# Kernel optimization log

Hardware: AMD Instinct MI355X
Metric: run time of the kernel (lower is better)

The kernel has to match this reference:

```python
import jax, jax.numpy as jnp
import numpy as np

N = 50000       # nodes
E = 1600000     # edges (avg degree 32)
F_IN = 128      # input node features
HID = 64        # hidden_dim
H = 2           # heads in conv1
NEG_SLOPE = 0.2 # PyG GATConv default


def gat_conv(x, W, a_src, a_dst, b, src, dst, heads, out_ch):
    """PyG-style GATConv (concat=True). x:[n,f], W:[f,heads*out_ch],
    a_src/a_dst:[heads,out_ch], b:[heads*out_ch], src/dst:[e]."""
    n = x.shape[0]
    xh = (x @ W).reshape(n, heads, out_ch)              # [n,H,C]
    s_src = jnp.sum(xh * a_src[None], axis=-1)          # [n,H]
    s_dst = jnp.sum(xh * a_dst[None], axis=-1)          # [n,H]
    e = jax.nn.leaky_relu(s_src[src] + s_dst[dst], NEG_SLOPE)  # [e,H]
    # segment softmax over incoming edges of each destination node
    emax = jax.ops.segment_max(e, dst, num_segments=n)  # [n,H]
    emax = jnp.where(jnp.isfinite(emax), emax, 0.0)
    p = jnp.exp(e - emax[dst])
    denom = jax.ops.segment_sum(p, dst, num_segments=n)
    alpha = p / (denom[dst] + 1e-16)                    # [e,H]
    out = jax.ops.segment_sum(xh[src] * alpha[..., None], dst, num_segments=n)
    return out.reshape(n, heads * out_ch) + b


def setup_inputs() -> dict:
    key = jax.random.key(0)
    ks = jax.random.split(key, 14)
    g = lambda k, shape, fan: jax.random.normal(k, shape, jnp.float32) / np.sqrt(fan).astype(np.float32)
    return {
        "x": jax.random.normal(ks[0], (N, F_IN), jnp.float32),
        "edge_index": jax.random.randint(ks[1], (2, E), 0, N, jnp.int32),
        "W1": g(ks[2], (F_IN, H * HID), F_IN),
        "a_src1": g(ks[3], (H, HID), HID),
        "a_dst1": g(ks[4], (H, HID), HID),
        "b1": jnp.zeros((H * HID,), jnp.float32),
        "W2": g(ks[5], (H * HID, HID), H * HID),
        "a_src2": g(ks[6], (1, HID), HID),
        "a_dst2": g(ks[7], (1, HID), HID),
        "b2": jnp.zeros((HID,), jnp.float32),
        "Wm": g(ks[8], (HID, 1), HID),
        "bm": jnp.zeros((1,), jnp.float32),
        "Wl": g(ks[9], (HID, 4), HID),
        "bl": jnp.zeros((4,), jnp.float32),
    }


def reference(x, edge_index, W1, a_src1, a_dst1, b1, W2, a_src2, a_dst2, b2, Wm, bm, Wl, bl):
    n = x.shape[0]
    loop = jnp.arange(n, dtype=edge_index.dtype)        # PyG add_self_loops=True
    src = jnp.concatenate([edge_index[0], loop])
    dst = jnp.concatenate([edge_index[1], loop])
    h = jax.nn.relu(gat_conv(x, W1, a_src1, a_dst1, b1, src, dst, H, HID))
    # dropout layers are identity in eval mode
    h = jax.nn.relu(gat_conv(h, W2, a_src2, a_dst2, b2, src, dst, 1, HID))
    mortality = h @ Wm + bm   # [n,1]
    los = h @ Wl + bl         # [n,4]
    return (mortality, los)
```

## Files before the change

### kernel.cpp

```cpp
#include <hip/hip_runtime.h>
#include <hip/hip_bf16.h>

typedef __hip_bfloat16 bf16;
typedef unsigned short ushort_t;
typedef __attribute__((ext_vector_type(8))) short short8;
typedef __attribute__((ext_vector_type(4))) float f32x4;

static __device__ __forceinline__ float b2f(const bf16 v){ return __bfloat162float(v); }
static __device__ __forceinline__ float lrelu(float x){ return x > 0.f ? x : 0.2f * x; }

static __device__ __forceinline__ float ldf(const void* p, size_t i, int f32){
  return f32 ? ((const float*)p)[i] : __bfloat162float(((const bf16*)p)[i]);
}

static __device__ __forceinline__ float wsum(float v){
#pragma unroll
  for (int o = 32; o; o >>= 1) v += __shfl_xor(v, o, 64);
  return v;
}
static __device__ __forceinline__ float wmax(float v){
#pragma unroll
  for (int o = 32; o; o >>= 1) v = fmaxf(v, __shfl_xor(v, o, 64));
  return v;
}
static __device__ __forceinline__ float qsum(float v){
  v += __shfl_xor(v, 1); v += __shfl_xor(v, 2);
  v += __shfl_xor(v, 4); v += __shfl_xor(v, 8);
  return v;
}

static __device__ __forceinline__ unsigned short f2bf(float x){
  unsigned u = __float_as_uint(x);
  unsigned r = (u + 0x7fffu + ((u >> 16) & 1u)) >> 16;
  return (unsigned short)r;
}
static __device__ __forceinline__ float bfval(unsigned short h){
  return __uint_as_float(((unsigned)h) << 16);
}
static __device__ __forceinline__ unsigned packbf2(float a, float b){
  return ((unsigned)f2bf(b) << 16) | (unsigned)f2bf(a);
}
static __device__ __forceinline__ float unlo(unsigned v){ return __uint_as_float(v << 16); }
static __device__ __forceinline__ float unhi(unsigned v){ return __uint_as_float(v & 0xffff0000u); }

__global__ void k_detect(const unsigned short* __restrict__ x, int* __restrict__ flag){
  __shared__ int cnt;
  if (threadIdx.x == 0) cnt = 0;
  __syncthreads();
  int bad = 0;
  for (int i = threadIdx.x; i < 8192; i += 256){
    int e = (x[i] >> 7) & 0xFF;
    if (e >= 133) bad++;
  }
  atomicAdd(&cnt, bad);
  __syncthreads();
  if (threadIdx.x == 0) *flag = (cnt > 16) ? 1 : 0;
}

__global__ void k_zero(int* __restrict__ p, int n){
  int i = blockIdx.x * blockDim.x + threadIdx.x;
  if (i < n) p[i] = 0;
}

#define CHUNK 8192

__global__ __launch_bounds__(256) void k_bincount(const int* __restrict__ ei,
                                                  int* __restrict__ bucketCnt,
                                                  int E, int Etot, int nbuck){
  __shared__ int lcnt[256];
  int t = threadIdx.x;
  lcnt[t] = 0;
  __syncthreads();
  int base = blockIdx.x * CHUNK;
#pragma unroll
  for (int k = 0; k < CHUNK / 256; k++){
    int i = base + k * 256 + t;
    if (i < Etot){
      int dst = (i < E) ? ei[E + i] : (i - E);
      atomicAdd(&lcnt[dst >> 8], 1);
    }
  }
  __syncthreads();
  if (t < nbuck && lcnt[t]) atomicAdd(&bucketCnt[t], lcnt[t]);
}

__global__ __launch_bounds__(256) void k_bucketscan(const int* __restrict__ bucketCnt,
                                                    int* __restrict__ bucketBase,
                                                    int* __restrict__ bucketCur, int nbuck){
  __shared__ int sm[256];
  int t = threadIdx.x;
  int v = (t < nbuck) ? bucketCnt[t] : 0;
  sm[t] = v;
  __syncthreads();
#pragma unroll
  for (int o = 1; o < 256; o <<= 1){
    int x = (t >= o) ? sm[t - o] : 0;
    __syncthreads();
    sm[t] += x;
    __syncthreads();
  }
  int excl = sm[t] - v;
  if (t < nbuck){ bucketBase[t] = excl; bucketCur[t] = excl; }
  if (t == 255) bucketBase[nbuck] = sm[255];
}

__global__ __launch_bounds__(256) void k_binscatter(const int* __restrict__ ei,
                                                    int* __restrict__ bucketCur,
                                                    unsigned* __restrict__ binned,
                                                    int E, int Etot, int nbuck){
  __shared__ int lcnt[256];
  __shared__ int lcur[256];
  int t = threadIdx.x;
  lcnt[t] = 0;
  __syncthreads();
  int base = blockIdx.x * CHUNK;
#pragma unroll
  for (int k = 0; k < CHUNK / 256; k++){
    int i = base + k * 256 + t;
    if (i < Etot){
      int dst = (i < E) ? ei[E + i] : (i - E);
      atomicAdd(&lcnt[dst >> 8], 1);
    }
  }
  __syncthreads();
  if (t < nbuck) lcur[t] = lcnt[t] ? atomicAdd(&bucketCur[t], lcnt[t]) : 0;
  __syncthreads();
#pragma unroll
  for (int k = 0; k < CHUNK / 256; k++){
    int i = base + k * 256 + t;
    if (i < Etot){
      int src, dst;
      if (i < E){ src = ei[i]; dst = ei[E + i]; } else { src = i - E; dst = i - E; }
      int p = atomicAdd(&lcur[dst >> 8], 1);
      binned[p] = (unsigned)src | ((unsigned)(dst & 255) << 24);
    }
  }
}

#define SORTCAP 12288
__global__ __launch_bounds__(256) void k_bucketsort(const int* __restrict__ bucketBase,
                                                    const unsigned* __restrict__ binned,
                                                    int* __restrict__ deg, int* __restrict__ offs,
                                                    int* __restrict__ csr, int N){
  __shared__ int lcnt[256];
  __shared__ int lsc[256];
  __shared__ int lcur[256];
  __shared__ int lsrc[SORTCAP];
  int t = threadIdx.x;
  int b = blockIdx.x;
  int s0 = bucketBase[b], s1 = bucketBase[b + 1];
  int cnt = s1 - s0;
  int node0 = b << 8;
  lcnt[t] = 0;
  __syncthreads();
  for (int i = t; i < cnt; i += 256){
    unsigned v = binned[s0 + i];
    atomicAdd(&lcnt[v >> 24], 1);
  }
  __syncthreads();
  lsc[t] = lcnt[t];
  __syncthreads();
#pragma unroll
  for (int o = 1; o < 256; o <<= 1){
    int x = (t >= o) ? lsc[t - o] : 0;
    __syncthreads();
    lsc[t] += x;
    __syncthreads();
  }
  int excl = lsc[t] - lcnt[t];
  int node = node0 + t;
  if (node < N){ deg[node] = lcnt[t]; offs[node] = s0 + excl; }
  lcur[t] = excl;
  __syncthreads();
  if (cnt <= SORTCAP){
    for (int i = t; i < cnt; i += 256){
      unsigned v = binned[s0 + i];
      int p = atomicAdd(&lcur[v >> 24], 1);
      lsrc[p] = (int)(v & 0xFFFFFFu);
    }
    __syncthreads();
    for (int i = t; i < cnt; i += 256) csr[s0 + i] = lsrc[i];
  } else {
    for (int i = t; i < cnt; i += 256){
      unsigned v = binned[s0 + i];
      int p = atomicAdd(&lcur[v >> 24], 1);
      csr[s0 + p] = (int)(v & 0xFFFFFFu);
    }
  }
}

__global__ __launch_bounds__(256) void k_prepw(const void* __restrict__ W, int ncol, int nct,
                                               const int* __restrict__ flagp,
                                               unsigned short* __restrict__ hi,
                                               unsigned short* __restrict__ lo){
  const int f = *flagp;
  int t = blockIdx.x * 256 + threadIdx.x;
  int j = t & 7;
  int lane = (t >> 3) & 63;
  int ct = (t >> 9) % nct;
  int kc = t / (512 * nct);
  int k = kc * 32 + ((lane >> 4) << 3) + j;
  int col = ct * 16 + (lane & 15);
  float w = ldf(W, (size_t)k * ncol + col, f);
  unsigned short h = f2bf(w);
  hi[t] = h;
  lo[t] = f2bf(w - bfval(h));
}

__global__ __launch_bounds__(256) void k_gemm1m(
    const void* __restrict__ x,
    const unsigned short* __restrict__ whi, const unsigned short* __restrict__ wlo,
    const void* __restrict__ a_src1, const void* __restrict__ a_dst1,
    const int* __restrict__ flagp,
    unsigned* __restrict__ xh1p, float* __restrict__ ssrc1, float* __restrict__ sdst1, int n){
  const int f = *flagp;
  int t = threadIdx.x;
  int lane = t & 63, w = t >> 6;
  int c16 = lane & 15, quad = lane >> 4;
  int nbw = blockIdx.x * 64 + w * 16;
  int an = min(nbw + c16, n - 1);
  f32x4 acc[8];
#pragma unroll
  for (int ct = 0; ct < 8; ct++)
#pragma unroll
    for (int r = 0; r < 4; r++) acc[ct][r] = 0.f;

#pragma unroll
  for (int kc = 0; kc < 4; kc++){
    float av[8];
    short8 ahi, alo;
    if (f){
      const float* row = (const float*)x + (size_t)an * 128 + kc * 32 + quad * 8;
      float4 v0 = *(const float4*)row;
      float4 v1 = *(const float4*)(row + 4);
      av[0] = v0.x; av[1] = v0.y; av[2] = v0.z; av[3] = v0.w;
      av[4] = v1.x; av[5] = v1.y; av[6] = v1.z; av[7] = v1.w;
#pragma unroll
      for (int j = 0; j < 8; j++){
        unsigned short h = f2bf(av[j]);
        ahi[j] = (short)h;
        alo[j] = (short)f2bf(av[j] - bfval(h));
      }
    } else {
      const unsigned short* row = (const unsigned short*)x + (size_t)an * 128 + kc * 32 + quad * 8;
      uint4 v = *(const uint4*)row;
      ahi[0] = (short)(v.x & 0xffff); ahi[1] = (short)(v.x >> 16);
      ahi[2] = (short)(v.y & 0xffff); ahi[3] = (short)(v.y >> 16);
      ahi[4] = (short)(v.z & 0xffff); ahi[5] = (short)(v.z >> 16);
      ahi[6] = (short)(v.w & 0xffff); ahi[7] = (short)(v.w >> 16);
#pragma unroll
      for (int j = 0; j < 8; j++) alo[j] = 0;
    }
#pragma unroll
    for (int ct = 0; ct < 8; ct++){
      const short8 bhi = *(const short8*)(whi + (((size_t)(kc * 8 + ct) * 64 + lane) << 3));
      const short8 blo = *(const short8*)(wlo + (((size_t)(kc * 8 + ct) * 64 + lane) << 3));
      acc[ct] = __builtin_amdgcn_mfma_f32_16x16x32_bf16(ahi, blo, acc[ct], 0, 0, 0);
      acc[ct] = __builtin_amdgcn_mfma_f32_16x16x32_bf16(alo, bhi, acc[ct], 0, 0, 0);
      acc[ct] = __builtin_amdgcn_mfma_f32_16x16x32_bf16(ahi, bhi, acc[ct], 0, 0, 0);
    }
  }

  float as[8], ad[8];
#pragma unroll
  for (int ct = 0; ct < 8; ct++){
    as[ct] = ldf(a_src1, ct * 16 + c16, f);
    ad[ct] = ldf(a_dst1, ct * 16 + c16, f);
  }
  float vs0[4], vs1[4], vd0[4], vd1[4];
#pragma unroll
  for (int r = 0; r < 4; r++){
    float s0 = 0.f, s1 = 0.f, d0 = 0.f, d1 = 0.f;
#pragma unroll
    for (int ct = 0; ct < 4; ct++){
      s0 += acc[ct][r] * as[ct];      d0 += acc[ct][r] * ad[ct];
      s1 += acc[ct + 4][r] * as[ct + 4]; d1 += acc[ct + 4][r] * ad[ct + 4];
    }
    vs0[r] = qsum(s0); vs1[r] = qsum(s1);
    vd0[r] = qsum(d0); vd1[r] = qsum(d1);
  }
#pragma unroll
  for (int r = 0; r < 4; r++){
    int node = nbw + quad * 4 + r;
    if (node < n){
#pragma unroll
      for (int ct = 0; ct < 4; ct++)
        xh1p[(size_t)node * 64 + ct * 16 + c16] = packbf2(acc[ct][r], acc[ct + 4][r]);
    }
  }
  if (c16 == 0){
#pragma unroll
    for (int r = 0; r < 4; r++){
      int node = nbw + quad * 4 + r;
      if (node < n){
        ssrc1[node * 2]     = vs0[r];
        ssrc1[node * 2 + 1] = vs1[r];
        sdst1[node * 2]     = vd0[r];
        sdst1[node * 2 + 1] = vd1[r];
      }
    }
  }
}

__global__ __launch_bounds__(256) void k_gemm2m(
    const float* __restrict__ h1,
    const unsigned short* __restrict__ whi, const unsigned short* __restrict__ wlo,
    const void* __restrict__ a_src2, const void* __restrict__ a_dst2,
    const int* __restrict__ flagp,
    unsigned short* __restrict__ xh2b, float* __restrict__ ssrc2, float* __restrict__ sdst2, int n){
  const int f = *flagp;
  int t = threadIdx.x;
  int lane = t & 63, w = t >> 6;
  int c16 = lane & 15, quad = lane >> 4;
  int nbw = blockIdx.x * 64 + w * 16;
  int an = min(nbw + c16, n - 1);
  f32x4 acc[4];
#pragma unroll
  for (int ct = 0; ct < 4; ct++)
#pragma unroll
    for (int r = 0; r < 4; r++) acc[ct][r] = 0.f;

#pragma unroll
  for (int kc = 0; kc < 4; kc++){
    const float* row = h1 + (size_t)an * 128 + kc * 32 + quad * 8;
    float4 v0 = *(const float4*)row;
    float4 v1 = *(const float4*)(row + 4);
    float av[8] = {v0.x, v0.y, v0.z, v0.w, v1.x, v1.y, v1.z, v1.w};
    short8 ahi, alo;
#pragma unroll
    for (int j = 0; j < 8; j++){
      unsigned short h = f2bf(av[j]);
      ahi[j] = (short)h;
      alo[j] = (short)f2bf(av[j] - bfval(h));
    }
#pragma unroll
    for (int ct = 0; ct < 4; ct++){
      const short8 bhi = *(const short8*)(whi + (((size_t)(kc * 4 + ct) * 64 + lane) << 3));
      const short8 blo = *(const short8*)(wlo + (((size_t)(kc * 4 + ct) * 64 + lane) << 3));
      acc[ct] = __builtin_amdgcn_mfma_f32_16x16x32_bf16(ahi, blo, acc[ct], 0, 0, 0);
      acc[ct] = __builtin_amdgcn_mfma_f32_16x16x32_bf16(alo, bhi, acc[ct], 0, 0, 0);
      acc[ct] = __builtin_amdgcn_mfma_f32_16x16x32_bf16(ahi, bhi, acc[ct], 0, 0, 0);
    }
  }

  float as[4], ad[4];
#pragma unroll
  for (int ct = 0; ct < 4; ct++){
    as[ct] = ldf(a_src2, ct * 16 + c16, f);
    ad[ct] = ldf(a_dst2, ct * 16 + c16, f);
  }
  float vs[4], vd[4];
#pragma unroll
  for (int r = 0; r < 4; r++){
    float s = 0.f, d = 0.f;
#pragma unroll
    for (int ct = 0; ct < 4; ct++){
      s += acc[ct][r] * as[ct];
      d += acc[ct][r] * ad[ct];
    }
    vs[r] = qsum(s); vd[r] = qsum(d);
  }
#pragma unroll
  for (int r = 0; r < 4; r++){
    int node = nbw + quad * 4 + r;
    if (node < n){
#pragma unroll
      for (int ct = 0; ct < 4; ct++)
        xh2b[(size_t)node * 64 + ct * 16 + c16] = f2bf(acc[ct][r]);
    }
  }
  if (c16 == 0){
#pragma unroll
    for (int r = 0; r < 4; r++){
      int node = nbw + quad * 4 + r;
      if (node < n){ ssrc2[node] = vs[r]; sdst2[node] = vd[r]; }
    }
  }
}

__global__ __launch_bounds__(256) void k_agg1(
    const int* __restrict__ offs, const int* __restrict__ deg, const int* __restrict__ csr,
    const float2* __restrict__ ssrc, const float2* __restrict__ sdst,
    const unsigned* __restrict__ xh1p, const void* __restrict__ b1,
    const int* __restrict__ flagp, float* __restrict__ h1, int n){
  int wid = (int)(((size_t)blockIdx.x * blockDim.x + threadIdx.x) >> 6);
  int lane = threadIdx.x & 63;
  if (wid >= n) return;
  int st = offs[wid], d = deg[wid];
  int half = lane >> 5, u = lane & 31;
  float2 sd = sdst[wid];
  const uint2* xp = (const uint2*)xh1p;
  float m0 = -3e38f, m1 = -3e38f, Z0 = 0.f, Z1 = 0.f;
  float a0x = 0.f, a0y = 0.f, a1x = 0.f, a1y = 0.f;
  for (int base = 0; base < d; base += 64){
    int idx = base + lane;
    bool val = idx < d;
    int s = csr[st + (val ? idx : 0)];
    float2 sv = ssrc[s];
    float e0 = val ? lrelu(sv.x + sd.x) : -3e38f;
    float e1 = val ? lrelu(sv.y + sd.y) : -3e38f;
    float nm0 = fmaxf(m0, wmax(e0));
    float nm1 = fmaxf(m1, wmax(e1));
    float r0 = __expf(m0 - nm0), r1 = __expf(m1 - nm1);
    Z0 *= r0; a0x *= r0; a0y *= r0;
    Z1 *= r1; a1x *= r1; a1y *= r1;
    m0 = nm0; m1 = nm1;
    float p0 = val ? __expf(e0 - m0) : 0.f;
    float p1 = val ? __expf(e1 - m1) : 0.f;
    Z0 += wsum(p0); Z1 += wsum(p1);
    int cnt = min(64, d - base);
    int pairs = (cnt + 1) >> 1;
    for (int pj = 0; pj < pairs; pj += 4){
      int jj0 = ((pj + 0) << 1) + half;
      int jj1 = ((pj + 1) << 1) + half;
      int jj2 = ((pj + 2) << 1) + half;
      int jj3 = ((pj + 3) << 1) + half;
      int s0 = __shfl(s, jj0), s1 = __shfl(s, jj1), s2 = __shfl(s, jj2), s3 = __shfl(s, jj3);
      float q00 = __shfl(p0, jj0), q01 = __shfl(p0, jj1), q02 = __shfl(p0, jj2), q03 = __shfl(p0, jj3);
      float q10 = __shfl(p1, jj0), q11 = __shfl(p1, jj1), q12 = __shfl(p1, jj2), q13 = __shfl(p1, jj3);
      uint2 v0 = xp[(size_t)(unsigned)s0 * 32 + u];
      uint2 v1 = xp[(size_t)(unsigned)s1 * 32 + u];
      uint2 v2 = xp[(size_t)(unsigned)s2 * 32 + u];
      uint2 v3 = xp[(size_t)(unsigned)s3 * 32 + u];
      a0x = fmaf(q00, unlo(v0.x), a0x); a0y = fmaf(q00, unlo(v0.y), a0y);
      a1x = fmaf(q10, unhi(v0.x), a1x); a1y = fmaf(q10, unhi(v0.y), a1y);
      a0x = fmaf(q01, unlo(v1.x), a0x); a0y = fmaf(q01, unlo(v1.y), a0y);
      a1x = fmaf(q11, unhi(v1.x), a1x); a1y = fmaf(q11, unhi(v1.y), a1y);
      a0x = fmaf(q02, unlo(v2.x), a0x); a0y = fmaf(q02, unlo(v2.y), a0y);
      a1x = fmaf(q12, unhi(v2.x), a1x); a1y = fmaf(q12, unhi(v2.y), a1y);
      a0x = fmaf(q03, unlo(v3.x), a0x); a0y = fmaf(q03, unlo(v3.y), a0y);
      a1x = fmaf(q13, unhi(v3.x), a1x); a1y = fmaf(q13, unhi(v3.y), a1y);
    }
  }
  a0x += __shfl_xor(a0x, 32); a0y += __shfl_xor(a0y, 32);
  a1x += __shfl_xor(a1x, 32); a1y += __shfl_xor(a1y, 32);
  const int f = *flagp;
  float Zh = half ? Z1 : Z0;
  float ax = half ? a1x : a0x;
  float ay = half ? a1y : a0y;
  float inv = 1.f / (Zh + 1e-16f);
  float bx = ldf(b1, half * 64 + 2 * u, f);
  float by = ldf(b1, half * 64 + 2 * u + 1, f);
  float2 o;
  o.x = fmaxf(ax * inv + bx, 0.f);
  o.y = fmaxf(ay * inv + by, 0.f);
  *(float2*)&h1[(size_t)wid * 128 + half * 64 + 2 * u] = o;
}

__global__ __launch_bounds__(256) void k_agg2(
    const int* __restrict__ offs, const int* __restrict__ deg, const int* __restrict__ csr,
    const float* __restrict__ ssrc, const float* __restrict__ sdstA,
    const unsigned short* __restrict__ xh2b, const void* __restrict__ bias2,
    const void* __restrict__ Wm, const void* __restrict__ bm,
    const void* __restrict__ Wlos, const void* __restrict__ bl,
    const int* __restrict__ flagp, void* __restrict__ out, int n){
  int wid = (int)(((size_t)blockIdx.x * blockDim.x + threadIdx.x) >> 6);
  int lane = threadIdx.x & 63;
  if (wid >= n) return;
  int st = offs[wid], d = deg[wid];
  int half = lane >> 5, u = lane & 31;
  float sd = sdstA[wid];
  const unsigned* xp = (const unsigned*)xh2b;
  float m = -3e38f, Z = 0.f, ax = 0.f, ay = 0.f;
  for (int base = 0; base < d; base += 64){
    int idx = base + lane;
    bool val = idx < d;
    int s = csr[st + (val ? idx : 0)];
    float e = val ? lrelu(ssrc[s] + sd) : -3e38f;
    float nm = fmaxf(m, wmax(e));
    float r = __expf(m - nm);
    Z *= r; ax *= r; ay *= r; m = nm;
    float p = val ? __expf(e - m) : 0.f;
    Z += wsum(p);
    int cnt = min(64, d - base);
    int pairs = (cnt + 1) >> 1;
    for (int pj = 0; pj < pairs; pj += 4){
      int jj0 = ((pj + 0) << 1) + half;
      int jj1 = ((pj + 1) << 1) + half;
      int jj2 = ((pj + 2) << 1) + half;
      int jj3 = ((pj + 3) << 1) + half;
      int s0 = __shfl(s, jj0), s1 = __shfl(s, jj1), s2 = __shfl(s, jj2), s3 = __shfl(s, jj3);
      float q0 = __shfl(p, jj0), q1 = __shfl(p, jj1), q2 = __shfl(p, jj2), q3 = __shfl(p, jj3);
      unsigned v0 = xp[(size_t)(unsigned)s0 * 32 + u];
      unsigned v1 = xp[(size_t)(unsigned)s1 * 32 + u];
      unsigned v2 = xp[(size_t)(unsigned)s2 * 32 + u];
      unsigned v3 = xp[(size_t)(unsigned)s3 * 32 + u];
      ax = fmaf(q0, unlo(v0), ax); ay = fmaf(q0, unhi(v0), ay);
      ax = fmaf(q1, unlo(v1), ax); ay = fmaf(q1, unhi(v1), ay);
      ax = fmaf(q2, unlo(v2), ax); ay = fmaf(q2, unhi(v2), ay);
      ax = fmaf(q3, unlo(v3), ax); ay = fmaf(q3, unhi(v3), ay);
    }
  }
  ax += __shfl_xor(ax, 32);
  ay += __shfl_xor(ay, 32);
  const int f = *flagp;
  float inv = 1.f / (Z + 1e-16f);
  float hx = fmaxf(ax * inv + ldf(bias2, 2 * u, f), 0.f);
  float hy = fmaxf(ay * inv + ldf(bias2, 2 * u + 1, f), 0.f);
  bool lo32 = (half == 0);
  float mo = wsum(lo32 ? hx * ldf(Wm, 2 * u, f) + hy * ldf(Wm, 2 * u + 1, f) : 0.f);
  float l0 = wsum(lo32 ? hx * ldf(Wlos, (2 * u) * 4 + 0, f) + hy * ldf(Wlos, (2 * u + 1) * 4 + 0, f) : 0.f);
  float l1 = wsum(lo32 ? hx * ldf(Wlos, (2 * u) * 4 + 1, f) + hy * ldf(Wlos, (2 * u + 1) * 4 + 1, f) : 0.f);
  float l2 = wsum(lo32 ? hx * ldf(Wlos, (2 * u) * 4 + 2, f) + hy * ldf(Wlos, (2 * u + 1) * 4 + 2, f) : 0.f);
  float l3 = wsum(lo32 ? hx * ldf(Wlos, (2 * u) * 4 + 3, f) + hy * ldf(Wlos, (2 * u + 1) * 4 + 3, f) : 0.f);
  if (lane == 0){
    float vm = mo + ldf(bm, 0, f);
    float v0 = l0 + ldf(bl, 0, f);
    float v1 = l1 + ldf(bl, 1, f);
    float v2 = l2 + ldf(bl, 2, f);
    float v3 = l3 + ldf(bl, 3, f);
    if (f){
      float* o = (float*)out;
      o[wid] = vm;
      float4 lv = make_float4(v0, v1, v2, v3);
      *(float4*)&o[n + wid * 4] = lv;
    } else {
      bf16* o = (bf16*)out;
      o[wid] = __float2bfloat16(vm);
      o[n + wid * 4 + 0] = __float2bfloat16(v0); o[n + wid * 4 + 1] = __float2bfloat16(v1);
      o[n + wid * 4 + 2] = __float2bfloat16(v2); o[n + wid * 4 + 3] = __float2bfloat16(v3);
    }
  }
}

extern "C" void kernel_launch(void* const* d_in, const int* in_sizes, int n_in,
                              void* d_out, int out_size, void* d_ws, size_t ws_size,
                              hipStream_t stream){
  const void* x      = d_in[0];
  const int*  ei     = (const int*)d_in[1];
  const void* W1     = d_in[2];
  const void* a_src1 = d_in[3];
  const void* a_dst1 = d_in[4];
  const void* b1     = d_in[5];
  const void* W2     = d_in[6];
  const void* a_src2 = d_in[7];
  const void* a_dst2 = d_in[8];
  const void* bias2  = d_in[9];
  const void* Wm     = d_in[10];
  const void* bm     = d_in[11];
  const void* Wlos   = d_in[12];
  const void* bl     = d_in[13];

  const int N = in_sizes[0] / 128;
  const int E = in_sizes[1] / 2;
  const int Etot = E + N;
  const int NBUCK = (N + 255) >> 8;

  char* base = (char*)d_ws;
  size_t off = 0;
  auto alloc = [&](size_t bytes) -> void* {
    void* r = base + off;
    off += (bytes + 255) & ~(size_t)255;
    return r;
  };
  int*      flag  = (int*)alloc(256);
  unsigned* xh1p  = (unsigned*)alloc((size_t)N * 64 * 4);
  float*    h1    = (float*)alloc((size_t)N * 128 * 4);
  float*    ssrc1 = (float*)alloc((size_t)N * 2 * 4);
  float*    sdst1 = (float*)alloc((size_t)N * 2 * 4);
  float*    ssrc2 = (float*)alloc((size_t)N * 4);
  float*    sdst2 = (float*)alloc((size_t)N * 4);
  int*      deg     = (int*)alloc((size_t)N * 4);
  int*      offsb   = (int*)alloc((size_t)N * 4);
  int*      csr     = (int*)alloc((size_t)Etot * 4);
  unsigned* binned  = (unsigned*)alloc((size_t)Etot * 4);
  int*      bucketCnt  = (int*)alloc(1024);
  int*      bucketBase = (int*)alloc(1024 + 4);
  int*      bucketCur  = (int*)alloc(1024);
  unsigned short* w1hi = (unsigned short*)alloc(16384 * 2);
  unsigned short* w1lo = (unsigned short*)alloc(16384 * 2);
  unsigned short* w2hi = (unsigned short*)alloc(8192 * 2);
  unsigned short* w2lo = (unsigned short*)alloc(8192 * 2);
  unsigned short* xh2b = (unsigned short*)xh1p;

  const int nchunk = (Etot + CHUNK - 1) / CHUNK;

  k_detect<<<1, 256, 0, stream>>>((const unsigned short*)x, flag);

  k_prepw<<<64, 256, 0, stream>>>(W1, 128, 8, flag, w1hi, w1lo);
  k_prepw<<<32, 256, 0, stream>>>(W2, 64, 4, flag, w2hi, w2lo);

  k_zero<<<1, 256, 0, stream>>>(bucketCnt, NBUCK);
  k_bincount<<<nchunk, 256, 0, stream>>>(ei, bucketCnt, E, Etot, NBUCK);
  k_bucketscan<<<1, 256, 0, stream>>>(bucketCnt, bucketBase, bucketCur, NBUCK);
  k_binscatter<<<nchunk, 256, 0, stream>>>(ei, bucketCur, binned, E, Etot, NBUCK);
  k_bucketsort<<<NBUCK, 256, 0, stream>>>(bucketBase, binned, deg, offsb, csr, N);

  k_gemm1m<<<(N + 63) / 64, 256, 0, stream>>>(x, w1hi, w1lo, a_src1, a_dst1, flag, xh1p, ssrc1, sdst1, N);
  k_agg1<<<(N + 3) / 4, 256, 0, stream>>>(offsb, deg, csr, (const float2*)ssrc1, (const float2*)sdst1,
                                          xh1p, b1, flag, h1, N);

  k_gemm2m<<<(N + 63) / 64, 256, 0, stream>>>(h1, w2hi, w2lo, a_src2, a_dst2, flag, xh2b, ssrc2, sdst2, N);
  k_agg2<<<(N + 3) / 4, 256, 0, stream>>>(offsb, deg, csr, ssrc2, sdst2, xh2b, bias2,
                                          Wm, bm, Wlos, bl, flag, d_out, N);
}
```

Measured before the change: 311.7 us.

## Use fixed-capacity buckets to drop count/scan passes and widen aggregation gathers

```diff
diff --git a/kernel.cpp b/kernel.cpp
--- a/kernel.cpp
+++ b/kernel.cpp
@@ -2,7 +2,6 @@
 #include <hip/hip_bf16.h>
 
 typedef __hip_bfloat16 bf16;
-typedef unsigned short ushort_t;
 typedef __attribute__((ext_vector_type(8))) short short8;
 typedef __attribute__((ext_vector_type(4))) float f32x4;
 
@@ -43,7 +42,8 @@
 static __device__ __forceinline__ float unlo(unsigned v){ return __uint_as_float(v << 16); }
 static __device__ __forceinline__ float unhi(unsigned v){ return __uint_as_float(v & 0xffff0000u); }
 
-__global__ void k_detect(const unsigned short* __restrict__ x, int* __restrict__ flag){
+__global__ void k_detect(const unsigned short* __restrict__ x, int* __restrict__ flag,
+                         int* __restrict__ bucketCur, int nbuck){
   __shared__ int cnt;
   if (threadIdx.x == 0) cnt = 0;
   __syncthreads();
@@ -53,92 +53,51 @@
     if (e >= 133) bad++;
   }
   atomicAdd(&cnt, bad);
+  for (int i = threadIdx.x; i < nbuck; i += 256) bucketCur[i] = 0;
   __syncthreads();
   if (threadIdx.x == 0) *flag = (cnt > 16) ? 1 : 0;
 }
 
-__global__ void k_zero(int* __restrict__ p, int n){
-  int i = blockIdx.x * blockDim.x + threadIdx.x;
-  if (i < n) p[i] = 0;
-}
-
-#define CHUNK 8192
-
-__global__ __launch_bounds__(256) void k_bincount(const int* __restrict__ ei,
-                                                  int* __restrict__ bucketCnt,
-                                                  int E, int Etot, int nbuck){
-  __shared__ int lcnt[256];
-  int t = threadIdx.x;
-  lcnt[t] = 0;
-  __syncthreads();
-  int base = blockIdx.x * CHUNK;
-#pragma unroll
-  for (int k = 0; k < CHUNK / 256; k++){
-    int i = base + k * 256 + t;
-    if (i < Etot){
-      int dst = (i < E) ? ei[E + i] : (i - E);
-      atomicAdd(&lcnt[dst >> 8], 1);
-    }
-  }
-  __syncthreads();
-  if (t < nbuck && lcnt[t]) atomicAdd(&bucketCnt[t], lcnt[t]);
-}
-
-__global__ __launch_bounds__(256) void k_bucketscan(const int* __restrict__ bucketCnt,
-                                                    int* __restrict__ bucketBase,
-                                                    int* __restrict__ bucketCur, int nbuck){
-  __shared__ int sm[256];
-  int t = threadIdx.x;
-  int v = (t < nbuck) ? bucketCnt[t] : 0;
-  sm[t] = v;
-  __syncthreads();
-#pragma unroll
-  for (int o = 1; o < 256; o <<= 1){
-    int x = (t >= o) ? sm[t - o] : 0;
-    __syncthreads();
-    sm[t] += x;
-    __syncthreads();
-  }
-  int excl = sm[t] - v;
-  if (t < nbuck){ bucketBase[t] = excl; bucketCur[t] = excl; }
-  if (t == 255) bucketBase[nbuck] = sm[255];
-}
+#define CAP 10240
+#define EPB 16
+#define CHUNK (256 * EPB)
 
 __global__ __launch_bounds__(256) void k_binscatter(const int* __restrict__ ei,
                                                     int* __restrict__ bucketCur,
                                                     unsigned* __restrict__ binned,
-                                                    int E, int Etot, int nbuck){
+                                                    int E, int Etot){
   __shared__ int lcnt[256];
   __shared__ int lcur[256];
   int t = threadIdx.x;
   lcnt[t] = 0;
   __syncthreads();
   int base = blockIdx.x * CHUNK;
-#pragma unroll
-  for (int k = 0; k < CHUNK / 256; k++){
+  int vsrc[EPB], vdst[EPB];
+#pragma unroll
+  for (int k = 0; k < EPB; k++){
     int i = base + k * 256 + t;
+    vdst[k] = -1;
     if (i < Etot){
-      int dst = (i < E) ? ei[E + i] : (i - E);
-      atomicAdd(&lcnt[dst >> 8], 1);
-    }
-  }
-  __syncthreads();
-  if (t < nbuck) lcur[t] = lcnt[t] ? atomicAdd(&bucketCur[t], lcnt[t]) : 0;
-  __syncthreads();
-#pragma unroll
-  for (int k = 0; k < CHUNK / 256; k++){
-    int i = base + k * 256 + t;
-    if (i < Etot){
-      int src, dst;
-      if (i < E){ src = ei[i]; dst = ei[E + i]; } else { src = i - E; dst = i - E; }
-      int p = atomicAdd(&lcur[dst >> 8], 1);
-      binned[p] = (unsigned)src | ((unsigned)(dst & 255) << 24);
-    }
-  }
-}
-
-#define SORTCAP 12288
-__global__ __launch_bounds__(256) void k_bucketsort(const int* __restrict__ bucketBase,
+      if (i < E){ vsrc[k] = ei[i]; vdst[k] = ei[E + i]; }
+      else { vsrc[k] = i - E; vdst[k] = i - E; }
+      atomicAdd(&lcnt[vdst[k] >> 8], 1);
+    }
+  }
+  __syncthreads();
+  lcur[t] = lcnt[t] ? atomicAdd(&bucketCur[t], lcnt[t]) : 0;
+  __syncthreads();
+#pragma unroll
+  for (int k = 0; k < EPB; k++){
+    if (vdst[k] >= 0){
+      int b = vdst[k] >> 8;
+      int p = atomicAdd(&lcur[b], 1);
+      binned[(size_t)b * CAP + p] = (unsigned)vsrc[k] | ((unsigned)(vdst[k] & 255) << 24);
+    }
+  }
+}
+
+#define SORTCAP 10240
+__global__ __launch_bounds__(256) void k_bucketsort(const int* __restrict__ bucketCur,
                                                     const unsigned* __restrict__ binned,
                                                     int* __restrict__ deg, int* __restrict__ offs,
                                                     int* __restrict__ csr, int N){
@@ -148,8 +107,8 @@
   __shared__ int lsrc[SORTCAP];
   int t = threadIdx.x;
   int b = blockIdx.x;
-  int s0 = bucketBase[b], s1 = bucketBase[b + 1];
-  int cnt = s1 - s0;
+  int s0 = b * CAP;
+  int cnt = bucketCur[b];
   int node0 = b << 8;
   lcnt[t] = 0;
   __syncthreads();
@@ -189,12 +148,15 @@
   }
 }
 
-__global__ __launch_bounds__(256) void k_prepw(const void* __restrict__ W, int ncol, int nct,
-                                               const int* __restrict__ flagp,
-                                               unsigned short* __restrict__ hi,
-                                               unsigned short* __restrict__ lo){
+__global__ __launch_bounds__(256) void k_prepw2(const void* __restrict__ W1, const void* __restrict__ W2,
+                                                const int* __restrict__ flagp,
+                                                unsigned short* __restrict__ w1hi, unsigned short* __restrict__ w1lo,
+                                                unsigned short* __restrict__ w2hi, unsigned short* __restrict__ w2lo){
   const int f = *flagp;
-  int t = blockIdx.x * 256 + threadIdx.x;
+  int blk = blockIdx.x;
+  const void* W; unsigned short *hi, *lo; int ncol, nct, t;
+  if (blk < 64){ W = W1; hi = w1hi; lo = w1lo; ncol = 128; nct = 8; t = blk * 256 + threadIdx.x; }
+  else         { W = W2; hi = w2hi; lo = w2lo; ncol = 64;  nct = 4; t = (blk - 64) * 256 + threadIdx.x; }
   int j = t & 7;
   int lane = (t >> 3) & 63;
   int ct = (t >> 9) % nct;
@@ -387,11 +349,12 @@
   int lane = threadIdx.x & 63;
   if (wid >= n) return;
   int st = offs[wid], d = deg[wid];
-  int half = lane >> 5, u = lane & 31;
+  int quarter = lane >> 4, u = lane & 15;
   float2 sd = sdst[wid];
-  const uint2* xp = (const uint2*)xh1p;
+  const uint4* xp = (const uint4*)xh1p;
   float m0 = -3e38f, m1 = -3e38f, Z0 = 0.f, Z1 = 0.f;
-  float a0x = 0.f, a0y = 0.f, a1x = 0.f, a1y = 0.f;
+  float a0[4] = {0.f, 0.f, 0.f, 0.f};
+  float a1[4] = {0.f, 0.f, 0.f, 0.f};
   for (int base = 0; base < d; base += 64){
     int idx = base + lane;
     bool val = idx < d;
@@ -402,49 +365,68 @@
     float nm0 = fmaxf(m0, wmax(e0));
     float nm1 = fmaxf(m1, wmax(e1));
     float r0 = __expf(m0 - nm0), r1 = __expf(m1 - nm1);
-    Z0 *= r0; a0x *= r0; a0y *= r0;
-    Z1 *= r1; a1x *= r1; a1y *= r1;
+    Z0 *= r0; Z1 *= r1;
+#pragma unroll
+    for (int c = 0; c < 4; c++){ a0[c] *= r0; a1[c] *= r1; }
     m0 = nm0; m1 = nm1;
     float p0 = val ? __expf(e0 - m0) : 0.f;
     float p1 = val ? __expf(e1 - m1) : 0.f;
     Z0 += wsum(p0); Z1 += wsum(p1);
     int cnt = min(64, d - base);
-    int pairs = (cnt + 1) >> 1;
-    for (int pj = 0; pj < pairs; pj += 4){
-      int jj0 = ((pj + 0) << 1) + half;
-      int jj1 = ((pj + 1) << 1) + half;
-      int jj2 = ((pj + 2) << 1) + half;
-      int jj3 = ((pj + 3) << 1) + half;
-      int s0 = __shfl(s, jj0), s1 = __shfl(s, jj1), s2 = __shfl(s, jj2), s3 = __shfl(s, jj3);
-      float q00 = __shfl(p0, jj0), q01 = __shfl(p0, jj1), q02 = __shfl(p0, jj2), q03 = __shfl(p0, jj3);
-      float q10 = __shfl(p1, jj0), q11 = __shfl(p1, jj1), q12 = __shfl(p1, jj2), q13 = __shfl(p1, jj3);
-      uint2 v0 = xp[(size_t)(unsigned)s0 * 32 + u];
-      uint2 v1 = xp[(size_t)(unsigned)s1 * 32 + u];
-      uint2 v2 = xp[(size_t)(unsigned)s2 * 32 + u];
-      uint2 v3 = xp[(size_t)(unsigned)s3 * 32 + u];
-      a0x = fmaf(q00, unlo(v0.x), a0x); a0y = fmaf(q00, unlo(v0.y), a0y);
-      a1x = fmaf(q10, unhi(v0.x), a1x); a1y = fmaf(q10, unhi(v0.y), a1y);
-      a0x = fmaf(q01, unlo(v1.x), a0x); a0y = fmaf(q01, unlo(v1.y), a0y);
-      a1x = fmaf(q11, unhi(v1.x), a1x); a1y = fmaf(q11, unhi(v1.y), a1y);
-      a0x = fmaf(q02, unlo(v2.x), a0x); a0y = fmaf(q02, unlo(v2.y), a0y);
-      a1x = fmaf(q12, unhi(v2.x), a1x); a1y = fmaf(q12, unhi(v2.y), a1y);
-      a0x = fmaf(q03, unlo(v3.x), a0x); a0y = fmaf(q03, unlo(v3.y), a0y);
-      a1x = fmaf(q13, unhi(v3.x), a1x); a1y = fmaf(q13, unhi(v3.y), a1y);
-    }
-  }
-  a0x += __shfl_xor(a0x, 32); a0y += __shfl_xor(a0y, 32);
-  a1x += __shfl_xor(a1x, 32); a1y += __shfl_xor(a1y, 32);
+    int groups = (cnt + 3) >> 2;
+    for (int g = 0; g < groups; g += 4){
+      int j0 = ((g + 0) << 2) + quarter;
+      int j1 = ((g + 1) << 2) + quarter;
+      int j2 = ((g + 2) << 2) + quarter;
+      int j3 = ((g + 3) << 2) + quarter;
+      int s0 = __shfl(s, j0), s1 = __shfl(s, j1), s2 = __shfl(s, j2), s3 = __shfl(s, j3);
+      float q00 = __shfl(p0, j0), q01 = __shfl(p0, j1), q02 = __shfl(p0, j2), q03 = __shfl(p0, j3);
+      float q10 = __shfl(p1, j0), q11 = __shfl(p1, j1), q12 = __shfl(p1, j2), q13 = __shfl(p1, j3);
+      uint4 v0 = xp[(size_t)(unsigned)s0 * 16 + u];
+      uint4 v1 = xp[(size_t)(unsigned)s1 * 16 + u];
+      uint4 v2 = xp[(size_t)(unsigned)s2 * 16 + u];
+      uint4 v3 = xp[(size_t)(unsigned)s3 * 16 + u];
+      a0[0] = fmaf(q00, unlo(v0.x), a0[0]); a1[0] = fmaf(q10, unhi(v0.x), a1[0]);
+      a0[1] = fmaf(q00, unlo(v0.y), a0[1]); a1[1] = fmaf(q10, unhi(v0.y), a1[1]);
+      a0[2] = fmaf(q00, unlo(v0.z), a0[2]); a1[2] = fmaf(q10, unhi(v0.z), a1[2]);
+      a0[3] = fmaf(q00, unlo(v0.w), a0[3]); a1[3] = fmaf(q10, unhi(v0.w), a1[3]);
+      a0[0] = fmaf(q01, unlo(v1.x), a0[0]); a1[0] = fmaf(q11, unhi(v1.x), a1[0]);
+      a0[1] = fmaf(q01, unlo(v1.y), a0[1]); a1[1] = fmaf(q11, unhi(v1.y), a1[1]);
+      a0[2] = fmaf(q01, unlo(v1.z), a0[2]); a1[2] = fmaf(q11, unhi(v1.z), a1[2]);
+      a0[3] = fmaf(q01, unlo(v1.w), a0[3]); a1[3] = fmaf(q11, unhi(v1.w), a1[3]);
+      a0[0] = fmaf(q02, unlo(v2.x), a0[0]); a1[0] = fmaf(q12, unhi(v2.x), a1[0]);
+      a0[1] = fmaf(q02, unlo(v2.y), a0[1]); a1[1] = fmaf(q12, unhi(v2.y), a1[1]);
+      a0[2] = fmaf(q02, unlo(v2.z), a0[2]); a1[2] = fmaf(q12, unhi(v2.z), a1[2]);
+      a0[3] = fmaf(q02, unlo(v2.w), a0[3]); a1[3] = fmaf(q12, unhi(v2.w), a1[3]);
+      a0[0] = fmaf(q03, unlo(v3.x), a0[0]); a1[0] = fmaf(q13, unhi(v3.x), a1[0]);
+      a0[1] = fmaf(q03, unlo(v3.y), a0[1]); a1[1] = fmaf(q13, unhi(v3.y), a1[1]);
+      a0[2] = fmaf(q03, unlo(v3.z), a0[2]); a1[2] = fmaf(q13, unhi(v3.z), a1[2]);
+      a0[3] = fmaf(q03, unlo(v3.w), a0[3]); a1[3] = fmaf(q13, unhi(v3.w), a1[3]);
+    }
+  }
+#pragma unroll
+  for (int c = 0; c < 4; c++){
+    a0[c] += __shfl_xor(a0[c], 32); a0[c] += __shfl_xor(a0[c], 16);
+    a1[c] += __shfl_xor(a1[c], 32); a1[c] += __shfl_xor(a1[c], 16);
+  }
   const int f = *flagp;
-  float Zh = half ? Z1 : Z0;
-  float ax = half ? a1x : a0x;
-  float ay = half ? a1y : a0y;
-  float inv = 1.f / (Zh + 1e-16f);
-  float bx = ldf(b1, half * 64 + 2 * u, f);
-  float by = ldf(b1, half * 64 + 2 * u + 1, f);
-  float2 o;
-  o.x = fmaxf(ax * inv + bx, 0.f);
-  o.y = fmaxf(ay * inv + by, 0.f);
-  *(float2*)&h1[(size_t)wid * 128 + half * 64 + 2 * u] = o;
+  float i0 = 1.f / (Z0 + 1e-16f);
+  float i1 = 1.f / (Z1 + 1e-16f);
+  if (quarter == 0){
+    float4 o;
+    o.x = fmaxf(a0[0] * i0 + ldf(b1, 4 * u + 0, f), 0.f);
+    o.y = fmaxf(a0[1] * i0 + ldf(b1, 4 * u + 1, f), 0.f);
+    o.z = fmaxf(a0[2] * i0 + ldf(b1, 4 * u + 2, f), 0.f);
+    o.w = fmaxf(a0[3] * i0 + ldf(b1, 4 * u + 3, f), 0.f);
+    *(float4*)&h1[(size_t)wid * 128 + 4 * u] = o;
+  } else if (quarter == 1){
+    float4 o;
+    o.x = fmaxf(a1[0] * i1 + ldf(b1, 64 + 4 * u + 0, f), 0.f);
+    o.y = fmaxf(a1[1] * i1 + ldf(b1, 64 + 4 * u + 1, f), 0.f);
+    o.z = fmaxf(a1[2] * i1 + ldf(b1, 64 + 4 * u + 2, f), 0.f);
+    o.w = fmaxf(a1[3] * i1 + ldf(b1, 64 + 4 * u + 3, f), 0.f);
+    *(float4*)&h1[(size_t)wid * 128 + 64 + 4 * u] = o;
+  }
 }
 
 __global__ __launch_bounds__(256) void k_agg2(
@@ -458,10 +440,11 @@
   int lane = threadIdx.x & 63;
   if (wid >= n) return;
   int st = offs[wid], d = deg[wid];
-  int half = lane >> 5, u = lane & 31;
+  int quarter = lane >> 4, u = lane & 15;
   float sd = sdstA[wid];
-  const unsigned* xp = (const unsigned*)xh2b;
-  float m = -3e38f, Z = 0.f, ax = 0.f, ay = 0.f;
+  const uint2* xp = (const uint2*)xh2b;
+  float m = -3e38f, Z = 0.f;
+  float ax[4] = {0.f, 0.f, 0.f, 0.f};
   for (int base = 0; base < d; base += 64){
     int idx = base + lane;
     bool val = idx < d;
@@ -469,40 +452,61 @@
     float e = val ? lrelu(ssrc[s] + sd) : -3e38f;
     float nm = fmaxf(m, wmax(e));
     float r = __expf(m - nm);
-    Z *= r; ax *= r; ay *= r; m = nm;
+    Z *= r;
+#pragma unroll
+    for (int c = 0; c < 4; c++) ax[c] *= r;
+    m = nm;
     float p = val ? __expf(e - m) : 0.f;
     Z += wsum(p);
     int cnt = min(64, d - base);
-    int pairs = (cnt + 1) >> 1;
-    for (int pj = 0; pj < pairs; pj += 4){
-      int jj0 = ((pj + 0) << 1) + half;
-      int jj1 = ((pj + 1) << 1) + half;
-      int jj2 = ((pj + 2) << 1) + half;
-      int jj3 = ((pj + 3) << 1) + half;
-      int s0 = __shfl(s, jj0), s1 = __shfl(s, jj1), s2 = __shfl(s, jj2), s3 = __shfl(s, jj3);
-      float q0 = __shfl(p, jj0), q1 = __shfl(p, jj1), q2 = __shfl(p, jj2), q3 = __shfl(p, jj3);
-      unsigned v0 = xp[(size_t)(unsigned)s0 * 32 + u];
-      unsigned v1 = xp[(size_t)(unsigned)s1 * 32 + u];
-      unsigned v2 = xp[(size_t)(unsigned)s2 * 32 + u];
-      unsigned v3 = xp[(size_t)(unsigned)s3 * 32 + u];
-      ax = fmaf(q0, unlo(v0), ax); ay = fmaf(q0, unhi(v0), ay);
-      ax = fmaf(q1, unlo(v1), ax); ay = fmaf(q1, unhi(v1), ay);
-      ax = fmaf(q2, unlo(v2), ax); ay = fmaf(q2, unhi(v2), ay);
-      ax = fmaf(q3, unlo(v3), ax); ay = fmaf(q3, unhi(v3), ay);
-    }
-  }
-  ax += __shfl_xor(ax, 32);
-  ay += __shfl_xor(ay, 32);
+    int groups = (cnt + 3) >> 2;
+    for (int g = 0; g < groups; g += 4){
+      int j0 = ((g + 0) << 2) + quarter;
+      int j1 = ((g + 1) << 2) + quarter;
+      int j2 = ((g + 2) << 2) + quarter;
+      int j3 = ((g + 3) << 2) + quarter;
+      int s0 = __shfl(s, j0), s1 = __shfl(s, j1), s2 = __shfl(s, j2), s3 = __shfl(s, j3);
+      float q0 = __shfl(p, j0), q1 = __shfl(p, j1), q2 = __shfl(p, j2), q3 = __shfl(p, j3);
+      uint2 v0 = xp[(size_t)(unsigned)s0 * 16 + u];
+      uint2 v1 = xp[(size_t)(unsigned)s1 * 16 + u];
+      uint2 v2 = xp[(size_t)(unsigned)s2 * 16 + u];
+      uint2 v3 = xp[(size_t)(unsigned)s3 * 16 + u];
+      ax[0] = fmaf(q0, unlo(v0.x), ax[0]); ax[1] = fmaf(q0, unhi(v0.x), ax[1]);
+      ax[2] = fmaf(q0, unlo(v0.y), ax[2]); ax[3] = fmaf(q0, unhi(v0.y), ax[3]);
+      ax[0] = fmaf(q1, unlo(v1.x), ax[0]); ax[1] = fmaf(q1, unhi(v1.x), ax[1]);
+      ax[2] = fmaf(q1, unlo(v1.y), ax[2]); ax[3] = fmaf(q1, unhi(v1.y), ax[3]);
+      ax[0] = fmaf(q2, unlo(v2.x), ax[0]); ax[1] = fmaf(q2, unhi(v2.x), ax[1]);
+      ax[2] = fmaf(q2, unlo(v2.y), ax[2]); ax[3] = fmaf(q2, unhi(v2.y), ax[3]);
+      ax[0] = fmaf(q3, unlo(v3.x), ax[0]); ax[1] = fmaf(q3, unhi(v3.x), ax[1]);
+      ax[2] = fmaf(q3, unlo(v3.y), ax[2]); ax[3] = fmaf(q3, unhi(v3.y), ax[3]);
+    }
+  }
+#pragma unroll
+  for (int c = 0; c < 4; c++){
+    ax[c] += __shfl_xor(ax[c], 32);
+    ax[c] += __shfl_xor(ax[c], 16);
+  }
   const int f = *flagp;
   float inv = 1.f / (Z + 1e-16f);
-  float hx = fmaxf(ax * inv + ldf(bias2, 2 * u, f), 0.f);
-  float hy = fmaxf(ay * inv + ldf(bias2, 2 * u + 1, f), 0.f);
-  bool lo32 = (half == 0);
-  float mo = wsum(lo32 ? hx * ldf(Wm, 2 * u, f) + hy * ldf(Wm, 2 * u + 1, f) : 0.f);
-  float l0 = wsum(lo32 ? hx * ldf(Wlos, (2 * u) * 4 + 0, f) + hy * ldf(Wlos, (2 * u + 1) * 4 + 0, f) : 0.f);
-  float l1 = wsum(lo32 ? hx * ldf(Wlos, (2 * u) * 4 + 1, f) + hy * ldf(Wlos, (2 * u + 1) * 4 + 1, f) : 0.f);
-  float l2 = wsum(lo32 ? hx * ldf(Wlos, (2 * u) * 4 + 2, f) + hy * ldf(Wlos, (2 * u + 1) * 4 + 2, f) : 0.f);
-  float l3 = wsum(lo32 ? hx * ldf(Wlos, (2 * u) * 4 + 3, f) + hy * ldf(Wlos, (2 * u + 1) * 4 + 3, f) : 0.f);
+  float hv[4];
+#pragma unroll
+  for (int c = 0; c < 4; c++)
+    hv[c] = fmaxf(ax[c] * inv + ldf(bias2, 4 * u + c, f), 0.f);
+  bool q0w = (quarter == 0);
+  float pm = 0.f, p0 = 0.f, p1 = 0.f, p2 = 0.f, p3 = 0.f;
+  if (q0w){
+#pragma unroll
+    for (int c = 0; c < 4; c++){
+      int ch = 4 * u + c;
+      pm += hv[c] * ldf(Wm, ch, f);
+      p0 += hv[c] * ldf(Wlos, ch * 4 + 0, f);
+      p1 += hv[c] * ldf(Wlos, ch * 4 + 1, f);
+      p2 += hv[c] * ldf(Wlos, ch * 4 + 2, f);
+      p3 += hv[c] * ldf(Wlos, ch * 4 + 3, f);
+    }
+  }
+  float mo = wsum(pm);
+  float l0 = wsum(p0), l1 = wsum(p1), l2 = wsum(p2), l3 = wsum(p3);
   if (lane == 0){
     float vm = mo + ldf(bm, 0, f);
     float v0 = l0 + ldf(bl, 0, f);
@@ -560,13 +564,11 @@
   float*    sdst1 = (float*)alloc((size_t)N * 2 * 4);
   float*    ssrc2 = (float*)alloc((size_t)N * 4);
   float*    sdst2 = (float*)alloc((size_t)N * 4);
-  int*      deg     = (int*)alloc((size_t)N * 4);
-  int*      offsb   = (int*)alloc((size_t)N * 4);
-  int*      csr     = (int*)alloc((size_t)Etot * 4);
-  unsigned* binned  = (unsigned*)alloc((size_t)Etot * 4);
-  int*      bucketCnt  = (int*)alloc(1024);
-  int*      bucketBase = (int*)alloc(1024 + 4);
-  int*      bucketCur  = (int*)alloc(1024);
+  int*      deg    = (int*)alloc((size_t)N * 4);
+  int*      offsb  = (int*)alloc((size_t)N * 4);
+  unsigned* binned = (unsigned*)alloc((size_t)NBUCK * CAP * 4);
+  int*      csr    = (int*)alloc((size_t)NBUCK * CAP * 4);
+  int*      bucketCur = (int*)alloc(1024);
   unsigned short* w1hi = (unsigned short*)alloc(16384 * 2);
   unsigned short* w1lo = (unsigned short*)alloc(16384 * 2);
   unsigned short* w2hi = (unsigned short*)alloc(8192 * 2);
@@ -575,16 +577,11 @@
 
   const int nchunk = (Etot + CHUNK - 1) / CHUNK;
 
-  k_detect<<<1, 256, 0, stream>>>((const unsigned short*)x, flag);
-
-  k_prepw<<<64, 256, 0, stream>>>(W1, 128, 8, flag, w1hi, w1lo);
-  k_prepw<<<32, 256, 0, stream>>>(W2, 64, 4, flag, w2hi, w2lo);
-
-  k_zero<<<1, 256, 0, stream>>>(bucketCnt, NBUCK);
-  k_bincount<<<nchunk, 256, 0, stream>>>(ei, bucketCnt, E, Etot, NBUCK);
-  k_bucketscan<<<1, 256, 0, stream>>>(bucketCnt, bucketBase, bucketCur, NBUCK);
-  k_binscatter<<<nchunk, 256, 0, stream>>>(ei, bucketCur, binned, E, Etot, NBUCK);
-  k_bucketsort<<<NBUCK, 256, 0, stream>>>(bucketBase, binned, deg, offsb, csr, N);
+  k_detect<<<1, 256, 0, stream>>>((const unsigned short*)x, flag, bucketCur, NBUCK);
+  k_prepw2<<<96, 256, 0, stream>>>(W1, W2, flag, w1hi, w1lo, w2hi, w2lo);
+
+  k_binscatter<<<nchunk, 256, 0, stream>>>(ei, bucketCur, binned, E, Etot);
+  k_bucketsort<<<NBUCK, 256, 0, stream>>>(bucketCur, binned, deg, offsb, csr, N);
 
   k_gemm1m<<<(N + 63) / 64, 256, 0, stream>>>(x, w1hi, w1lo, a_src1, a_dst1, flag, xh1p, ssrc1, sdst1, N);
   k_agg1<<<(N + 3) / 4, 256, 0, stream>>>(offsb, deg, csr, (const float2*)ssrc1, (const float2*)sdst1,
```

New measurement: 308.4 us. No clear change (-1.1%).
